# Kernel tuning notes

Measured on AMD Instinct MI355X. Metric: run time of the kernel, lower is better.

## Reference

```python
import jax, jax.numpy as jnp
import numpy as np

N, E, G = 50000, 800000, 64
H, C, EDIM = 4, 64, 16
NT, NR, NCLS = 8, 6, 2
NEG_SLOPE = 0.2


def setup_inputs() -> dict:
    key = jax.random.key(0)
    ks = jax.random.split(key, 24)
    d = {}
    d['node_type'] = jax.random.randint(ks[0], (N,), 0, NT, dtype=jnp.int32)
    d['edge_type'] = jax.random.randint(ks[1], (E,), 0, NR, dtype=jnp.int32)
    d['edge_index'] = jax.random.randint(ks[2], (2, E), 0, N, dtype=jnp.int32)
    d['batch'] = jnp.sort(jax.random.randint(ks[3], (N,), 0, G, dtype=jnp.int32))
    i = [4]
    def rn(shape, scale=0.1):
        a = jax.random.normal(ks[i[0]], shape, dtype=jnp.float32) * scale
        i[0] += 1
        return a
    d['node_emb'] = rn((NT, C))
    d['edge_emb'] = rn((NR, EDIM))
    for l in (0, 1):
        d[f'W{l}'] = rn((C, H * C))
        d[f'We{l}'] = rn((EDIM, H * C))
        d[f'att_src{l}'] = rn((H, C))
        d[f'att_dst{l}'] = rn((H, C))
        d[f'att_edge{l}'] = rn((H, C))
        d[f'b{l}'] = jnp.zeros((C,), jnp.float32)
    d['cw1'] = rn((C, C))
    d['cb1'] = jnp.zeros((C,), jnp.float32)
    d['cw2'] = rn((C, NCLS))
    d['cb2'] = jnp.zeros((NCLS,), jnp.float32)
    return d


def gat_layer(x, ea, src, dst, W, We, a_src, a_dst, a_edge, b):
    # x: [N, C], ea: [E, EDIM]
    h = (x @ W).reshape(N, H, C)          # transformed node features
    he = (ea @ We).reshape(E, H, C)       # transformed edge features
    # per-edge attention logits [E, H]
    alpha = ((h * a_src).sum(-1)[src]
             + (h * a_dst).sum(-1)[dst]
             + (he * a_edge).sum(-1))
    alpha = jax.nn.leaky_relu(alpha, NEG_SLOPE)
    # segment softmax over destination neighborhoods
    m = jax.ops.segment_max(alpha, dst, num_segments=N)
    alpha = jnp.exp(alpha - m[dst])
    den = jax.ops.segment_sum(alpha, dst, num_segments=N)
    alpha = alpha / (den[dst] + 1e-16)
    # weighted scatter-add of source features, then mean over heads
    out = jax.ops.segment_sum(alpha[:, :, None] * h[src], dst, num_segments=N)
    return jax.nn.elu(out.mean(axis=1) + b)


def reference(node_type, edge_type, edge_index, batch, node_emb, edge_emb,
              W0, We0, att_src0, att_dst0, att_edge0, b0,
              W1, We1, att_src1, att_dst1, att_edge1, b1,
              cw1, cb1, cw2, cb2):
    src, dst = edge_index[0], edge_index[1]
    x = node_emb[node_type]          # [N, C]
    ea = edge_emb[edge_type]         # [E, EDIM]
    x = gat_layer(x, ea, src, dst, W0, We0, att_src0, att_dst0, att_edge0, b0)
    x = gat_layer(x, ea, src, dst, W1, We1, att_src1, att_dst1, att_edge1, b1)
    # global mean pool over graphs
    s = jax.ops.segment_sum(x, batch, num_segments=G)
    cnt = jax.ops.segment_sum(jnp.ones((N, 1), x.dtype), batch, num_segments=G)
    g = s / jnp.maximum(cnt, 1.0)
    # classifier (dropout inactive in eval)
    return jax.nn.relu(g @ cw1 + cb1) @ cw2 + cb2
```

## Files before the change

kernel.cpp:

```cpp
#include <hip/hip_runtime.h>
#include <hip/hip_bf16.h>

#define N_NODES 50000
#define N_EDGES 800000
#define N_GRAPH 64
#define NHEAD 4
#define CDIM 64
#define HC 256
#define NTT 8
#define NRR 6
#define EDIMM 16
#define SCAN_CHUNK 1024
#define NBLK_SCAN ((N_NODES + SCAN_CHUNK - 1) / SCAN_CHUNK)
#define H1SCALE 1024.f

typedef unsigned short u16;
typedef unsigned char u8;
typedef __attribute__((ext_vector_type(8))) short bf8;
typedef __attribute__((ext_vector_type(4))) float f4;
typedef __attribute__((ext_vector_type(2))) float v2f;

__device__ __forceinline__ float eluf(float v) { return v > 0.f ? v : expm1f(v); }
__device__ __forceinline__ u16 f2u(float f) {
    union { float f; unsigned int i; } c; c.f = f;
    unsigned int i = c.i;
    return (u16)((i + 0x7FFFu + ((i >> 16) & 1u)) >> 16);
}
__device__ __forceinline__ float lrelu(float v) { return v > 0.f ? v : 0.2f * v; }
__device__ __forceinline__ u8 f2fp8(float v) {
    return (u8)(__builtin_amdgcn_cvt_pk_fp8_f32(v, 0.f, 0, false) & 0xFF);
}

__global__ __launch_bounds__(256) void k_zero(float* __restrict__ p, int n)
{
    int i = blockIdx.x * 256 + threadIdx.x;
    if (i < n) p[i] = 0.f;
}

__global__ __launch_bounds__(256) void k_tables(
    const float* __restrict__ node_emb, const float* __restrict__ edge_emb,
    const float* __restrict__ W0, const float* __restrict__ We0,
    const float* __restrict__ as0, const float* __restrict__ ad0,
    const float* __restrict__ ae0, const float* __restrict__ We1,
    const float* __restrict__ ae1,
    float* __restrict__ t_h0, float* __restrict__ t_as0,
    float* __restrict__ t_ad0, float* __restrict__ t_ae0,
    float* __restrict__ t_ae1)
{
    __shared__ float srow[HC];
    __shared__ float srow2[HC];
    int tid = threadIdx.x;
    int b = blockIdx.x;
    if (b < NTT) {
        int t = b;
        float acc = 0.f;
        #pragma unroll 8
        for (int k = 0; k < CDIM; k++)
            acc += node_emb[t * CDIM + k] * W0[k * HC + tid];
        srow[tid] = acc;
        t_h0[t * HC + tid] = acc;
        __syncthreads();
        if (tid < NHEAD) {
            int h = tid;
            float a = 0.f, d = 0.f;
            for (int c = 0; c < CDIM; c++) {
                float hv = srow[h * CDIM + c];
                a += hv * as0[h * CDIM + c];
                d += hv * ad0[h * CDIM + c];
            }
            t_as0[t * NHEAD + h] = a;
            t_ad0[t * NHEAD + h] = d;
        }
    } else {
        int r = b - NTT;
        float a0 = 0.f, a1 = 0.f;
        #pragma unroll
        for (int k = 0; k < EDIMM; k++) {
            float ev = edge_emb[r * EDIMM + k];
            a0 += ev * We0[k * HC + tid];
            a1 += ev * We1[k * HC + tid];
        }
        srow[tid] = a0;
        srow2[tid] = a1;
        __syncthreads();
        if (tid < NHEAD) {
            int h = tid;
            float s0 = 0.f, s1 = 0.f;
            for (int c = 0; c < CDIM; c++) {
                s0 += srow[h * CDIM + c] * ae0[h * CDIM + c];
                s1 += srow2[h * CDIM + c] * ae1[h * CDIM + c];
            }
            t_ae0[r * NHEAD + h] = s0;
            t_ae1[r * NHEAD + h] = s1;
        }
    }
}

__global__ __launch_bounds__(256) void k_exptab(
    const float* __restrict__ t_as0, const float* __restrict__ t_ad0,
    const float* __restrict__ t_ae0, float* __restrict__ t_exp)
{
    for (int idx = threadIdx.x; idx < NTT * NRR * NTT * NHEAD; idx += 256) {
        int tn = idx / 192;
        int rem = idx - tn * 192;
        int et = rem >> 5;
        int ts = (rem >> 2) & 7;
        int h = rem & 3;
        float lg = t_as0[ts * NHEAD + h] + t_ad0[tn * NHEAD + h]
                 + t_ae0[et * NHEAD + h];
        t_exp[idx] = __expf(lrelu(lg));
    }
}

__global__ __launch_bounds__(256) void k_count(
    const int* __restrict__ edge_index, int* __restrict__ deg4,
    const int* __restrict__ batch, int* __restrict__ goffs)
{
    int i = blockIdx.x * 256 + threadIdx.x;
    if (i < N_EDGES)
        atomicAdd(&deg4[(blockIdx.x & 3) * N_NODES + edge_index[N_EDGES + i]], 1);
    if (i < N_NODES) {
        int bi = batch[i];
        int bp = (i == 0) ? -1 : batch[i - 1];
        for (int g = bp + 1; g <= bi; g++) goffs[g] = i;
        if (i == N_NODES - 1)
            for (int g = bi + 1; g <= N_GRAPH; g++) goffs[g] = N_NODES;
    }
}

__global__ __launch_bounds__(256) void k_scan1(
    const int* __restrict__ deg4, int* __restrict__ deg, int* __restrict__ blksum)
{
    __shared__ int s[256];
    int b = blockIdx.x, tid = threadIdx.x;
    int base = b * SCAN_CHUNK + tid * 4;
    int t = 0;
    #pragma unroll
    for (int k = 0; k < 4; k++) {
        int i = base + k;
        if (i < N_NODES) {
            int d = deg4[i] + deg4[N_NODES + i] + deg4[2 * N_NODES + i]
                  + deg4[3 * N_NODES + i];
            deg[i] = d;
            t += d;
        }
    }
    s[tid] = t;
    __syncthreads();
    for (int off = 128; off > 0; off >>= 1) {
        if (tid < off) s[tid] += s[tid + off];
        __syncthreads();
    }
    if (tid == 0) blksum[b] = s[0];
}

__global__ __launch_bounds__(256) void k_scan3(
    const int* __restrict__ deg, const int* __restrict__ blksum,
    int* __restrict__ offs, int* __restrict__ cursor)
{
    __shared__ int s[256];
    __shared__ int sbase;
    int b = blockIdx.x, tid = threadIdx.x;
    if (tid < 64) {
        int v = (tid < b) ? blksum[tid] : 0;
        #pragma unroll
        for (int d = 32; d >= 1; d >>= 1) v += __shfl_xor(v, d);
        if (tid == 0) sbase = v;
    }
    int base = b * SCAN_CHUNK + tid * 4;
    int d4[4]; int t = 0;
    #pragma unroll
    for (int k = 0; k < 4; k++) {
        int i = base + k;
        d4[k] = (i < N_NODES) ? deg[i] : 0;
        t += d4[k];
    }
    s[tid] = t;
    __syncthreads();
    for (int off = 1; off < 256; off <<= 1) {
        int v = (tid >= off) ? s[tid - off] : 0;
        __syncthreads();
        s[tid] += v;
        __syncthreads();
    }
    int excl = sbase + s[tid] - t;
    #pragma unroll
    for (int k = 0; k < 4; k++) {
        int i = base + k;
        if (i < N_NODES) { offs[i] = excl; cursor[i] = excl; }
        excl += d4[k];
    }
    if (b == NBLK_SCAN - 1 && tid == 255) offs[N_NODES] = excl;
}

__global__ __launch_bounds__(256) void k_scatter(
    const int* __restrict__ edge_index, const int* __restrict__ edge_type,
    const int* __restrict__ node_type, int* __restrict__ cursor,
    int* __restrict__ csrp)
{
    int e = blockIdx.x * 256 + threadIdx.x;
    if (e < N_EDGES) {
        int d  = edge_index[N_EDGES + e];
        int s  = edge_index[e];
        int et = edge_type[e];
        int ts = node_type[s];
        int pos = atomicAdd(&cursor[d], 1);
        csrp[pos] = s | (et << 16) | (ts << 19);
    }
}

__global__ __launch_bounds__(256) void k_layer0(
    const int* __restrict__ node_type, const int* __restrict__ offs,
    const int* __restrict__ csrp,
    const float* __restrict__ t_h0, const float* __restrict__ t_exp,
    const float* __restrict__ b0, u16* __restrict__ x1b)
{
    __shared__ float s_h0[NTT * HC];
    __shared__ float s_exp[NTT * NRR * NTT * NHEAD];
    __shared__ float s_b0[CDIM];

    int tid = threadIdx.x;
    for (int i = tid; i < NTT * HC; i += 256) s_h0[i] = t_h0[i];
    for (int i = tid; i < NTT * NRR * NTT * NHEAD; i += 256) s_exp[i] = t_exp[i];
    if (tid < CDIM) s_b0[tid] = b0[tid];
    __syncthreads();

    int n = (blockIdx.x * 256 + tid) >> 6;
    int lane = tid & 63;
    int h = lane >> 4;
    int cq = (lane & 15) << 2;
    int hoff = h * CDIM + cq;

    int tnbase = node_type[n] * 192 + h;
    int e0 = offs[n], e1 = offs[n + 1];
    int efull = e0 + ((e1 - e0) & ~3);
    float ax = 0.f, ay = 0.f, az = 0.f, aw = 0.f, den = 0.f;
    for (int i = e0; i < efull; i += 4) {
        int rA = csrp[i],     rB = csrp[i + 1];
        int rC = csrp[i + 2], rD = csrp[i + 3];
        int tA = rA >> 19, tB = rB >> 19, tC = rC >> 19, tD = rD >> 19;
        int eA = (rA >> 16) & 7, eB = (rB >> 16) & 7;
        int eC = (rC >> 16) & 7, eD = (rD >> 16) & 7;
        float pA = s_exp[tnbase + (eA << 5) + (tA << 2)];
        float pB = s_exp[tnbase + (eB << 5) + (tB << 2)];
        float pC = s_exp[tnbase + (eC << 5) + (tC << 2)];
        float pD = s_exp[tnbase + (eD << 5) + (tD << 2)];
        den += pA + pB + pC + pD;
        const float4 vA = *(const float4*)(s_h0 + tA * HC + hoff);
        const float4 vB = *(const float4*)(s_h0 + tB * HC + hoff);
        const float4 vC = *(const float4*)(s_h0 + tC * HC + hoff);
        const float4 vD = *(const float4*)(s_h0 + tD * HC + hoff);
        ax += pA * vA.x + pB * vB.x + pC * vC.x + pD * vD.x;
        ay += pA * vA.y + pB * vB.y + pC * vC.y + pD * vD.y;
        az += pA * vA.z + pB * vB.z + pC * vC.z + pD * vD.z;
        aw += pA * vA.w + pB * vB.w + pC * vC.w + pD * vD.w;
    }
    for (int i = efull; i < e1; i++) {
        int r = csrp[i];
        int ts = r >> 19, et = (r >> 16) & 7;
        float p = s_exp[tnbase + (et << 5) + (ts << 2)];
        den += p;
        const float4 v = *(const float4*)(s_h0 + ts * HC + hoff);
        ax += p * v.x; ay += p * v.y; az += p * v.z; aw += p * v.w;
    }
    float inv = 0.25f / (den + 1e-16f);
    ax *= inv; ay *= inv; az *= inv; aw *= inv;
    ax += __shfl_xor(ax, 16); ax += __shfl_xor(ax, 32);
    ay += __shfl_xor(ay, 16); ay += __shfl_xor(ay, 32);
    az += __shfl_xor(az, 16); az += __shfl_xor(az, 32);
    aw += __shfl_xor(aw, 16); aw += __shfl_xor(aw, 32);
    if (lane < 16) {
        ushort4 o;
        o.x = f2u(eluf(ax + s_b0[cq + 0]));
        o.y = f2u(eluf(ay + s_b0[cq + 1]));
        o.z = f2u(eluf(az + s_b0[cq + 2]));
        o.w = f2u(eluf(aw + s_b0[cq + 3]));
        *(ushort4*)(x1b + (size_t)n * CDIM + cq) = o;
    }
}

__global__ __launch_bounds__(256) void k_gemm1(
    const u16* __restrict__ x1b, const float* __restrict__ W1,
    const float* __restrict__ as1, const float* __restrict__ ad1,
    u8* __restrict__ h1f8, float* __restrict__ asrc1, float* __restrict__ adst1)
{
    __shared__ u8 ht[16 * HC];
    int tid = threadIdx.x;
    int lane = tid & 63, wv = tid >> 6;
    int quad = lane >> 4, c16 = lane & 15;

    bf8 bf[4][2];
    float sv[4], dv[4];
    #pragma unroll
    for (int t = 0; t < 4; t++) {
        int col = wv * 64 + t * 16 + c16;
        sv[t] = as1[col];
        dv[t] = ad1[col];
        #pragma unroll
        for (int kf = 0; kf < 2; kf++)
            #pragma unroll
            for (int j = 0; j < 8; j++)
                bf[t][kf][j] = (short)f2u(W1[(kf * 32 + quad * 8 + j) * HC + col]);
    }

    for (int it = 0; it < 5; it++) {
        int nt = it * 625 + blockIdx.x;
        const bf8 a0 = *(const bf8*)(x1b + (size_t)(nt * 16 + c16) * CDIM + quad * 8);
        const bf8 a1 = *(const bf8*)(x1b + (size_t)(nt * 16 + c16) * CDIM + 32 + quad * 8);
        f4 acc[4];
        #pragma unroll
        for (int t = 0; t < 4; t++) {
            acc[t] = (f4){0.f, 0.f, 0.f, 0.f};
            acc[t] = __builtin_amdgcn_mfma_f32_16x16x32_bf16(a0, bf[t][0], acc[t], 0, 0, 0);
            acc[t] = __builtin_amdgcn_mfma_f32_16x16x32_bf16(a1, bf[t][1], acc[t], 0, 0, 0);
        }
        float rs[4] = {0.f, 0.f, 0.f, 0.f}, rd[4] = {0.f, 0.f, 0.f, 0.f};
        #pragma unroll
        for (int t = 0; t < 4; t++)
            #pragma unroll
            for (int reg = 0; reg < 4; reg++) {
                float v = acc[t][reg];
                rs[reg] += v * sv[t];
                rd[reg] += v * dv[t];
                ht[(quad * 4 + reg) * HC + wv * 64 + t * 16 + c16] = f2fp8(v * H1SCALE);
            }
        #pragma unroll
        for (int reg = 0; reg < 4; reg++)
            #pragma unroll
            for (int d = 1; d < 16; d <<= 1) {
                rs[reg] += __shfl_xor(rs[reg], d);
                rd[reg] += __shfl_xor(rd[reg], d);
            }
        if (c16 == 0) {
            #pragma unroll
            for (int reg = 0; reg < 4; reg++) {
                int n = nt * 16 + quad * 4 + reg;
                asrc1[n * NHEAD + wv] = rs[reg];
                adst1[n * NHEAD + wv] = rd[reg];
            }
        }
        __syncthreads();
        const uint4* src = (const uint4*)ht;
        uint4* dst = (uint4*)(h1f8 + (size_t)nt * 16 * HC);
        dst[tid] = src[tid];
        __syncthreads();
    }
}

__global__ __launch_bounds__(256) void k_agg1(
    const int* __restrict__ offs, const int* __restrict__ csrp,
    const u8* __restrict__ h1f8, const float* __restrict__ asrc1,
    const float* __restrict__ adst1, const float* __restrict__ t_ae1,
    const float* __restrict__ b1, float* __restrict__ x2)
{
    __shared__ float s_ae[NRR * NHEAD];
    if (threadIdx.x < NRR * NHEAD) s_ae[threadIdx.x] = t_ae1[threadIdx.x];
    __syncthreads();

    int n = (blockIdx.x * 256 + threadIdx.x) >> 6;
    int lane = threadIdx.x & 63;
    int h = lane >> 4;
    int cq = (lane & 15) << 2;
    float adst = adst1[n * NHEAD + h];
    int e0 = offs[n], e1 = offs[n + 1];
    int efull = e0 + ((e1 - e0) & ~7);

    float ax = 0.f, ay = 0.f, az = 0.f, aw = 0.f, den = 0.f;
    for (int i = e0; i < efull; i += 8) {
        int rec[8], s[8], et[8];
        #pragma unroll
        for (int k = 0; k < 8; k++) rec[k] = csrp[i + k];
        #pragma unroll
        for (int k = 0; k < 8; k++) { s[k] = rec[k] & 0xFFFF; et[k] = (rec[k] >> 16) & 7; }
        float asv[8];
        unsigned int hw[8];
        #pragma unroll
        for (int k = 0; k < 8; k++) asv[k] = asrc1[s[k] * NHEAD + h];
        #pragma unroll
        for (int k = 0; k < 8; k++)
            hw[k] = *(const unsigned int*)(h1f8 + (size_t)s[k] * HC + h * CDIM + cq);
        #pragma unroll
        for (int k = 0; k < 8; k++) {
            float p = __expf(lrelu(asv[k] + adst + s_ae[et[k] * NHEAD + h]));
            den += p;
            v2f lo = __builtin_amdgcn_cvt_pk_f32_fp8(hw[k], false);
            v2f hi = __builtin_amdgcn_cvt_pk_f32_fp8(hw[k], true);
            ax += p * lo.x; ay += p * lo.y;
            az += p * hi.x; aw += p * hi.y;
        }
    }
    for (int i = efull; i < e1; i++) {
        int rec = csrp[i];
        int s = rec & 0xFFFF, et = (rec >> 16) & 7;
        float p = __expf(lrelu(asrc1[s * NHEAD + h] + adst + s_ae[et * NHEAD + h]));
        den += p;
        unsigned int w = *(const unsigned int*)(h1f8 + (size_t)s * HC + h * CDIM + cq);
        v2f lo = __builtin_amdgcn_cvt_pk_f32_fp8(w, false);
        v2f hi = __builtin_amdgcn_cvt_pk_f32_fp8(w, true);
        ax += p * lo.x; ay += p * lo.y;
        az += p * hi.x; aw += p * hi.y;
    }
    float inv = (0.25f / H1SCALE) / (den + 1e-16f);
    ax *= inv; ay *= inv; az *= inv; aw *= inv;
    ax += __shfl_xor(ax, 16); ax += __shfl_xor(ax, 32);
    ay += __shfl_xor(ay, 16); ay += __shfl_xor(ay, 32);
    az += __shfl_xor(az, 16); az += __shfl_xor(az, 32);
    aw += __shfl_xor(aw, 16); aw += __shfl_xor(aw, 32);
    if (lane < 16) {
        float4 o;
        o.x = eluf(ax + b1[cq + 0]);
        o.y = eluf(ay + b1[cq + 1]);
        o.z = eluf(az + b1[cq + 2]);
        o.w = eluf(aw + b1[cq + 3]);
        *(float4*)(x2 + (size_t)n * CDIM + cq) = o;
    }
}

__global__ __launch_bounds__(256) void k_poolcls(
    const float* __restrict__ x2, const int* __restrict__ goffs,
    const float* __restrict__ cw1, const float* __restrict__ cb1,
    const float* __restrict__ cw2, const float* __restrict__ cb2,
    float* __restrict__ out, int wsMB,
    const int* __restrict__ offs, const int* __restrict__ csrp,
    const float* __restrict__ W1)
{
    __shared__ float part[4][CDIM];
    __shared__ float gsh[CDIM];
    int g = blockIdx.x;
    int ch = threadIdx.x & 63, rg = threadIdx.x >> 6;
    int gs = goffs[g], ge = goffs[g + 1];
    float acc = 0.f;
    for (int r = gs + rg; r < ge; r += 4)
        acc += x2[(size_t)r * CDIM + ch];
    part[rg][ch] = acc;
    __syncthreads();
    if (threadIdx.x < CDIM) {
        float s = part[0][ch] + part[1][ch] + part[2][ch] + part[3][ch];
        int c = ge - gs;
        gsh[ch] = s / (float)(c > 1 ? c : 1);
    }
    __syncthreads();
    if (threadIdx.x < 64) {
        int j = threadIdx.x;
        float a = cb1[j];
        #pragma unroll
        for (int k = 0; k < CDIM; k++) a += gsh[k] * cw1[k * CDIM + j];
        float hid = a > 0.f ? a : 0.f;
        float o0 = hid * cw2[j * 2 + 0];
        float o1 = hid * cw2[j * 2 + 1];
        #pragma unroll
        for (int d = 32; d >= 1; d >>= 1) {
            o0 += __shfl_xor(o0, d);
            o1 += __shfl_xor(o1, d);
        }
        if (j == 0) {
            out[g * 2 + 0] = o0 + cb2[0];
            out[g * 2 + 1] = o1 + cb2[1];
        }
    }
    if (g == 0) {
        __shared__ int simpl, soob, sA;
        if (threadIdx.x == 0) { simpl = 0; soob = 0; sA = 0; }
        __syncthreads();
        if (threadIdx.x == 0 && offs[N_NODES] != N_EDGES) atomicOr(&sA, 4);
        float v = W1[threadIdx.x];
        if (!(fabsf(v) < 100.f)) atomicAdd(&simpl, 1);
        int r = csrp[threadIdx.x];
        if ((r & 0xFFFF) >= N_NODES || (r >> 22) != 0 || r < 0) atomicAdd(&soob, 1);
        __syncthreads();
        if (threadIdx.x == 0) {
            int A = sA;
            if (simpl > 10) A |= 8;
            int B = soob > 1023 ? 1023 : soob;
            if (A | B) out[0] = (float)((A << 20) | (wsMB << 10) | B);
        }
    }
}

__global__ void k_fault(int code, float* __restrict__ out)
{
    if (threadIdx.x == 0 && blockIdx.x == 0) out[0] = (float)code;
}

extern "C" void kernel_launch(void* const* d_in, const int* in_sizes, int n_in,
                              void* d_out, int out_size, void* d_ws, size_t ws_size,
                              hipStream_t stream) {
    static const int rsize[22] = {50000, 800000, 1600000, 50000, 512, 96,
                                  16384, 4096, 256, 256, 256, 64,
                                  16384, 4096, 256, 256, 256, 64,
                                  4096, 64, 128, 2};
    static const int cand_pos[3][22] = {
        {21,19,18,12,20,17,0,2,8,4,6,10,1,3,9,5,7,11,15,13,16,14},
        {0,1,2,3,4,5,6,7,8,9,10,11,12,13,14,15,16,17,18,19,20,21},
        {17,15,14,8,16,13,18,20,4,0,2,6,19,21,5,1,3,7,11,9,12,10},
    };
    int mc = -1;
    if (n_in == 22) {
        for (int c = 0; c < 3 && mc < 0; c++) {
            bool ok = true;
            for (int r = 0; r < 22; r++)
                if (in_sizes[cand_pos[c][r]] != rsize[r]) { ok = false; break; }
            if (ok) mc = c;
        }
    }

    char* ws = (char*)d_ws;
    size_t off = 0;
    auto alloc = [&](size_t b) { size_t r = off; off += (b + 255) & ~(size_t)255; return r; };
    int*   deg4   = (int*)(ws + alloc((size_t)4 * N_NODES * 4));
    size_t zero_bytes = off;
    int*   deg    = (int*)(ws + alloc(N_NODES * 4));
    int*   blksum = (int*)(ws + alloc(NBLK_SCAN * 4));
    int*   offs   = (int*)(ws + alloc((N_NODES + 1) * 4));
    int*   cursor = (int*)(ws + alloc(N_NODES * 4));
    int*   csrp   = (int*)(ws + alloc(N_EDGES * 4));
    int*   goffs  = (int*)(ws + alloc((N_GRAPH + 1) * 4));
    float* t_h0   = (float*)(ws + alloc(NTT * HC * 4));
    float* t_as0  = (float*)(ws + alloc(NTT * NHEAD * 4));
    float* t_ad0  = (float*)(ws + alloc(NTT * NHEAD * 4));
    float* t_ae0  = (float*)(ws + alloc(NRR * NHEAD * 4));
    float* t_ae1  = (float*)(ws + alloc(NRR * NHEAD * 4));
    float* t_exp  = (float*)(ws + alloc(NTT * NRR * NTT * NHEAD * 4));
    u16*   x1b    = (u16*)(ws + alloc((size_t)N_NODES * CDIM * 2));
    float* asrc1  = (float*)(ws + alloc((size_t)N_NODES * NHEAD * 4));
    float* adst1  = (float*)(ws + alloc((size_t)N_NODES * NHEAD * 4));
    u8*    h1f8   = (u8*)(ws + alloc((size_t)N_NODES * HC));
    float* x2     = (float*)(ws + alloc((size_t)N_NODES * CDIM * 4));

    int wsMB = (int)(ws_size >> 20); if (wsMB > 1023) wsMB = 1023;
    int hostA = 0, hostB = 0;
    if (mc < 0) { hostA |= 1; hostB = (n_in != 22) ? (n_in < 1023 ? n_in : 1023) : 0; }
    if (mc >= 0 && off > ws_size) hostA |= 2;

    if (hostA == 0) {
        const int* P = cand_pos[mc];
        const int*   node_type  = (const int*)d_in[P[0]];
        const int*   edge_type  = (const int*)d_in[P[1]];
        const int*   edge_index = (const int*)d_in[P[2]];
        const int*   batch      = (const int*)d_in[P[3]];
        const float* node_emb   = (const float*)d_in[P[4]];
        const float* edge_emb   = (const float*)d_in[P[5]];
        const float* W0  = (const float*)d_in[P[6]];
        const float* We0 = (const float*)d_in[P[7]];
        const float* as0 = (const float*)d_in[P[8]];
        const float* ad0 = (const float*)d_in[P[9]];
        const float* ae0 = (const float*)d_in[P[10]];
        const float* b0  = (const float*)d_in[P[11]];
        const float* W1  = (const float*)d_in[P[12]];
        const float* We1 = (const float*)d_in[P[13]];
        const float* as1 = (const float*)d_in[P[14]];
        const float* ad1 = (const float*)d_in[P[15]];
        const float* ae1 = (const float*)d_in[P[16]];
        const float* b1  = (const float*)d_in[P[17]];
        const float* cw1 = (const float*)d_in[P[18]];
        const float* cb1 = (const float*)d_in[P[19]];
        const float* cw2 = (const float*)d_in[P[20]];
        const float* cb2 = (const float*)d_in[P[21]];

        int zero_elems = (int)(zero_bytes / 4);
        k_zero<<<(zero_elems + 255) / 256, 256, 0, stream>>>((float*)ws, zero_elems);
        k_tables<<<NTT + NRR, 256, 0, stream>>>(node_emb, edge_emb, W0, We0, as0,
                                                ad0, ae0, We1, ae1,
                                                t_h0, t_as0, t_ad0, t_ae0, t_ae1);
        k_exptab<<<1, 256, 0, stream>>>(t_as0, t_ad0, t_ae0, t_exp);
        k_count<<<(N_EDGES + 255) / 256, 256, 0, stream>>>(edge_index, deg4,
                                                           batch, goffs);
        k_scan1<<<NBLK_SCAN, 256, 0, stream>>>(deg4, deg, blksum);
        k_scan3<<<NBLK_SCAN, 256, 0, stream>>>(deg, blksum, offs, cursor);
        k_scatter<<<(N_EDGES + 255) / 256, 256, 0, stream>>>(edge_index, edge_type,
                                                             node_type, cursor, csrp);
        k_layer0<<<(N_NODES * 64) / 256, 256, 0, stream>>>(
            node_type, offs, csrp, t_h0, t_exp, b0, x1b);
        k_gemm1<<<625, 256, 0, stream>>>(
            x1b, W1, as1, ad1, h1f8, asrc1, adst1);
        k_agg1<<<(N_NODES * 64) / 256, 256, 0, stream>>>(
            offs, csrp, h1f8, asrc1, adst1, t_ae1, b1, x2);
        k_poolcls<<<N_GRAPH, 256, 0, stream>>>(
            x2, goffs, cw1, cb1, cw2, cb2, (float*)d_out, wsMB, offs, csrp, W1);
    } else {
        int code = (hostA << 20) | (wsMB << 10) | (hostB > 1023 ? 1023 : hostB);
        k_fault<<<1, 64, 0, stream>>>(code, (float*)d_out);
    }
}
```

Before: 348.7 us.

## Fuse exp table into layer0, prefetch CSR records, distribute attention exps across lanes

Result: no change. 354.8 us (+1.8%).

```diff
diff --git a/kernel.cpp b/kernel.cpp
--- a/kernel.cpp
+++ b/kernel.cpp
@@ -96,22 +96,6 @@
     }
 }
 
-__global__ __launch_bounds__(256) void k_exptab(
-    const float* __restrict__ t_as0, const float* __restrict__ t_ad0,
-    const float* __restrict__ t_ae0, float* __restrict__ t_exp)
-{
-    for (int idx = threadIdx.x; idx < NTT * NRR * NTT * NHEAD; idx += 256) {
-        int tn = idx / 192;
-        int rem = idx - tn * 192;
-        int et = rem >> 5;
-        int ts = (rem >> 2) & 7;
-        int h = rem & 3;
-        float lg = t_as0[ts * NHEAD + h] + t_ad0[tn * NHEAD + h]
-                 + t_ae0[et * NHEAD + h];
-        t_exp[idx] = __expf(lrelu(lg));
-    }
-}
-
 __global__ __launch_bounds__(256) void k_count(
     const int* __restrict__ edge_index, int* __restrict__ deg4,
     const int* __restrict__ batch, int* __restrict__ goffs)
@@ -212,17 +196,35 @@
 __global__ __launch_bounds__(256) void k_layer0(
     const int* __restrict__ node_type, const int* __restrict__ offs,
     const int* __restrict__ csrp,
-    const float* __restrict__ t_h0, const float* __restrict__ t_exp,
+    const float* __restrict__ t_h0,
+    const float* __restrict__ t_as0, const float* __restrict__ t_ad0,
+    const float* __restrict__ t_ae0,
     const float* __restrict__ b0, u16* __restrict__ x1b)
 {
     __shared__ float s_h0[NTT * HC];
     __shared__ float s_exp[NTT * NRR * NTT * NHEAD];
     __shared__ float s_b0[CDIM];
+    __shared__ float s_att[2 * NTT * NHEAD + NRR * NHEAD];
 
     int tid = threadIdx.x;
     for (int i = tid; i < NTT * HC; i += 256) s_h0[i] = t_h0[i];
-    for (int i = tid; i < NTT * NRR * NTT * NHEAD; i += 256) s_exp[i] = t_exp[i];
+    if (tid < NTT * NHEAD) s_att[tid] = t_as0[tid];
+    else if (tid < 2 * NTT * NHEAD) s_att[tid] = t_ad0[tid - NTT * NHEAD];
+    else if (tid < 2 * NTT * NHEAD + NRR * NHEAD)
+        s_att[tid] = t_ae0[tid - 2 * NTT * NHEAD];
     if (tid < CDIM) s_b0[tid] = b0[tid];
+    __syncthreads();
+    for (int idx = tid; idx < NTT * NRR * NTT * NHEAD; idx += 256) {
+        int tn = idx / 192;
+        int rem = idx - tn * 192;
+        int et = rem >> 5;
+        int ts = (rem >> 2) & 7;
+        int hq = idx & 3;
+        float lg = s_att[ts * NHEAD + hq]
+                 + s_att[NTT * NHEAD + tn * NHEAD + hq]
+                 + s_att[2 * NTT * NHEAD + et * NHEAD + hq];
+        s_exp[idx] = __expf(lrelu(lg));
+    }
     __syncthreads();
 
     int n = (blockIdx.x * 256 + tid) >> 6;
@@ -233,35 +235,37 @@
 
     int tnbase = node_type[n] * 192 + h;
     int e0 = offs[n], e1 = offs[n + 1];
-    int efull = e0 + ((e1 - e0) & ~3);
+    int nb = (e1 - e0 + 7) >> 3;
     float ax = 0.f, ay = 0.f, az = 0.f, aw = 0.f, den = 0.f;
-    for (int i = e0; i < efull; i += 4) {
-        int rA = csrp[i],     rB = csrp[i + 1];
-        int rC = csrp[i + 2], rD = csrp[i + 3];
-        int tA = rA >> 19, tB = rB >> 19, tC = rC >> 19, tD = rD >> 19;
-        int eA = (rA >> 16) & 7, eB = (rB >> 16) & 7;
-        int eC = (rC >> 16) & 7, eD = (rD >> 16) & 7;
-        float pA = s_exp[tnbase + (eA << 5) + (tA << 2)];
-        float pB = s_exp[tnbase + (eB << 5) + (tB << 2)];
-        float pC = s_exp[tnbase + (eC << 5) + (tC << 2)];
-        float pD = s_exp[tnbase + (eD << 5) + (tD << 2)];
-        den += pA + pB + pC + pD;
-        const float4 vA = *(const float4*)(s_h0 + tA * HC + hoff);
-        const float4 vB = *(const float4*)(s_h0 + tB * HC + hoff);
-        const float4 vC = *(const float4*)(s_h0 + tC * HC + hoff);
-        const float4 vD = *(const float4*)(s_h0 + tD * HC + hoff);
-        ax += pA * vA.x + pB * vB.x + pC * vC.x + pD * vD.x;
-        ay += pA * vA.y + pB * vB.y + pC * vC.y + pD * vD.y;
-        az += pA * vA.z + pB * vB.z + pC * vC.z + pD * vD.z;
-        aw += pA * vA.w + pB * vB.w + pC * vC.w + pD * vD.w;
-    }
-    for (int i = efull; i < e1; i++) {
-        int r = csrp[i];
-        int ts = r >> 19, et = (r >> 16) & 7;
-        float p = s_exp[tnbase + (et << 5) + (ts << 2)];
-        den += p;
-        const float4 v = *(const float4*)(s_h0 + ts * HC + hoff);
-        ax += p * v.x; ay += p * v.y; az += p * v.z; aw += p * v.w;
+
+    int rec[8];
+    if (nb > 0) {
+        #pragma unroll
+        for (int k = 0; k < 8; k++) {
+            int idx = e0 + k; idx = idx < e1 ? idx : e1 - 1;
+            rec[k] = csrp[idx];
+        }
+    }
+    for (int b = 0; b < nb; b++) {
+        int i = e0 + (b << 3);
+        int lim = e1 - i;
+        int ts8[8], et8[8];
+        #pragma unroll
+        for (int k = 0; k < 8; k++) { ts8[k] = rec[k] >> 19; et8[k] = (rec[k] >> 16) & 7; }
+        int ii = i + 8;
+        #pragma unroll
+        for (int k = 0; k < 8; k++) {
+            int idx = ii + k; idx = idx < e1 ? idx : e1 - 1;
+            rec[k] = csrp[idx];
+        }
+        #pragma unroll
+        for (int k = 0; k < 8; k++) {
+            float p = s_exp[tnbase + (et8[k] << 5) + (ts8[k] << 2)];
+            p = (k < lim) ? p : 0.f;
+            den += p;
+            const float4 v = *(const float4*)(s_h0 + ts8[k] * HC + hoff);
+            ax += p * v.x; ay += p * v.y; az += p * v.z; aw += p * v.w;
+        }
     }
     float inv = 0.25f / (den + 1e-16f);
     ax *= inv; ay *= inv; az *= inv; aw *= inv;
@@ -303,48 +307,45 @@
                 bf[t][kf][j] = (short)f2u(W1[(kf * 32 + quad * 8 + j) * HC + col]);
     }
 
-    for (int it = 0; it < 5; it++) {
-        int nt = it * 625 + blockIdx.x;
-        const bf8 a0 = *(const bf8*)(x1b + (size_t)(nt * 16 + c16) * CDIM + quad * 8);
-        const bf8 a1 = *(const bf8*)(x1b + (size_t)(nt * 16 + c16) * CDIM + 32 + quad * 8);
-        f4 acc[4];
-        #pragma unroll
-        for (int t = 0; t < 4; t++) {
-            acc[t] = (f4){0.f, 0.f, 0.f, 0.f};
-            acc[t] = __builtin_amdgcn_mfma_f32_16x16x32_bf16(a0, bf[t][0], acc[t], 0, 0, 0);
-            acc[t] = __builtin_amdgcn_mfma_f32_16x16x32_bf16(a1, bf[t][1], acc[t], 0, 0, 0);
-        }
-        float rs[4] = {0.f, 0.f, 0.f, 0.f}, rd[4] = {0.f, 0.f, 0.f, 0.f};
-        #pragma unroll
-        for (int t = 0; t < 4; t++)
-            #pragma unroll
-            for (int reg = 0; reg < 4; reg++) {
-                float v = acc[t][reg];
-                rs[reg] += v * sv[t];
-                rd[reg] += v * dv[t];
-                ht[(quad * 4 + reg) * HC + wv * 64 + t * 16 + c16] = f2fp8(v * H1SCALE);
-            }
-        #pragma unroll
-        for (int reg = 0; reg < 4; reg++)
-            #pragma unroll
-            for (int d = 1; d < 16; d <<= 1) {
-                rs[reg] += __shfl_xor(rs[reg], d);
-                rd[reg] += __shfl_xor(rd[reg], d);
-            }
-        if (c16 == 0) {
-            #pragma unroll
-            for (int reg = 0; reg < 4; reg++) {
-                int n = nt * 16 + quad * 4 + reg;
-                asrc1[n * NHEAD + wv] = rs[reg];
-                adst1[n * NHEAD + wv] = rd[reg];
-            }
-        }
-        __syncthreads();
-        const uint4* src = (const uint4*)ht;
-        uint4* dst = (uint4*)(h1f8 + (size_t)nt * 16 * HC);
-        dst[tid] = src[tid];
-        __syncthreads();
-    }
+    int nt = blockIdx.x;
+    const bf8 a0 = *(const bf8*)(x1b + (size_t)(nt * 16 + c16) * CDIM + quad * 8);
+    const bf8 a1 = *(const bf8*)(x1b + (size_t)(nt * 16 + c16) * CDIM + 32 + quad * 8);
+    f4 acc[4];
+    #pragma unroll
+    for (int t = 0; t < 4; t++) {
+        acc[t] = (f4){0.f, 0.f, 0.f, 0.f};
+        acc[t] = __builtin_amdgcn_mfma_f32_16x16x32_bf16(a0, bf[t][0], acc[t], 0, 0, 0);
+        acc[t] = __builtin_amdgcn_mfma_f32_16x16x32_bf16(a1, bf[t][1], acc[t], 0, 0, 0);
+    }
+    float rs[4] = {0.f, 0.f, 0.f, 0.f}, rd[4] = {0.f, 0.f, 0.f, 0.f};
+    #pragma unroll
+    for (int t = 0; t < 4; t++)
+        #pragma unroll
+        for (int reg = 0; reg < 4; reg++) {
+            float v = acc[t][reg];
+            rs[reg] += v * sv[t];
+            rd[reg] += v * dv[t];
+            ht[(quad * 4 + reg) * HC + wv * 64 + t * 16 + c16] = f2fp8(v * H1SCALE);
+        }
+    #pragma unroll
+    for (int reg = 0; reg < 4; reg++)
+        #pragma unroll
+        for (int d = 1; d < 16; d <<= 1) {
+            rs[reg] += __shfl_xor(rs[reg], d);
+            rd[reg] += __shfl_xor(rd[reg], d);
+        }
+    if (c16 == 0) {
+        #pragma unroll
+        for (int reg = 0; reg < 4; reg++) {
+            int nn = nt * 16 + quad * 4 + reg;
+            asrc1[nn * NHEAD + wv] = rs[reg];
+            adst1[nn * NHEAD + wv] = rd[reg];
+        }
+    }
+    __syncthreads();
+    const uint4* src = (const uint4*)ht;
+    uint4* dst = (uint4*)(h1f8 + (size_t)nt * 16 * HC);
+    dst[tid] = src[tid];
 }
 
 __global__ __launch_bounds__(256) void k_agg1(
@@ -361,44 +362,53 @@
     int lane = threadIdx.x & 63;
     int h = lane >> 4;
     int cq = (lane & 15) << 2;
-    float adst = adst1[n * NHEAD + h];
+    int q  = lane & 31;
+    int ke = q >> 2;
+    int hh = q & 3;
+    float adst_hh = adst1[n * NHEAD + hh];
+
     int e0 = offs[n], e1 = offs[n + 1];
-    int efull = e0 + ((e1 - e0) & ~7);
+    int nb = (e1 - e0 + 7) >> 3;
 
     float ax = 0.f, ay = 0.f, az = 0.f, aw = 0.f, den = 0.f;
-    for (int i = e0; i < efull; i += 8) {
-        int rec[8], s[8], et[8];
-        #pragma unroll
-        for (int k = 0; k < 8; k++) rec[k] = csrp[i + k];
-        #pragma unroll
-        for (int k = 0; k < 8; k++) { s[k] = rec[k] & 0xFFFF; et[k] = (rec[k] >> 16) & 7; }
-        float asv[8];
+
+    int rec[8];
+    if (nb > 0) {
+        #pragma unroll
+        for (int k = 0; k < 8; k++) {
+            int idx = e0 + k; idx = idx < e1 ? idx : e1 - 1;
+            rec[k] = csrp[idx];
+        }
+    }
+    for (int b = 0; b < nb; b++) {
+        int i = e0 + (b << 3);
+        int lim = e1 - i;
+        int s[8];
+        #pragma unroll
+        for (int k = 0; k < 8; k++) s[k] = rec[k] & 0xFFFF;
+        int ete = (rec[ke] >> 16) & 7;
+        float asve = asrc1[s[ke] * NHEAD + hh];
         unsigned int hw[8];
-        #pragma unroll
-        for (int k = 0; k < 8; k++) asv[k] = asrc1[s[k] * NHEAD + h];
         #pragma unroll
         for (int k = 0; k < 8; k++)
             hw[k] = *(const unsigned int*)(h1f8 + (size_t)s[k] * HC + h * CDIM + cq);
+        int ii = i + 8;
         #pragma unroll
         for (int k = 0; k < 8; k++) {
-            float p = __expf(lrelu(asv[k] + adst + s_ae[et[k] * NHEAD + h]));
+            int idx = ii + k; idx = idx < e1 ? idx : e1 - 1;
+            rec[k] = csrp[idx];
+        }
+        float pe = __expf(lrelu(asve + adst_hh + s_ae[ete * NHEAD + hh]));
+        #pragma unroll
+        for (int k = 0; k < 8; k++) {
+            float p = __shfl(pe, (k << 2) | h);
+            p = (k < lim) ? p : 0.f;
             den += p;
             v2f lo = __builtin_amdgcn_cvt_pk_f32_fp8(hw[k], false);
             v2f hi = __builtin_amdgcn_cvt_pk_f32_fp8(hw[k], true);
             ax += p * lo.x; ay += p * lo.y;
             az += p * hi.x; aw += p * hi.y;
         }
-    }
-    for (int i = efull; i < e1; i++) {
-        int rec = csrp[i];
-        int s = rec & 0xFFFF, et = (rec >> 16) & 7;
-        float p = __expf(lrelu(asrc1[s * NHEAD + h] + adst + s_ae[et * NHEAD + h]));
-        den += p;
-        unsigned int w = *(const unsigned int*)(h1f8 + (size_t)s * HC + h * CDIM + cq);
-        v2f lo = __builtin_amdgcn_cvt_pk_f32_fp8(w, false);
-        v2f hi = __builtin_amdgcn_cvt_pk_f32_fp8(w, true);
-        ax += p * lo.x; ay += p * lo.y;
-        az += p * hi.x; aw += p * hi.y;
     }
     float inv = (0.25f / H1SCALE) / (den + 1e-16f);
     ax *= inv; ay *= inv; az *= inv; aw *= inv;
@@ -520,7 +530,6 @@
     float* t_ad0  = (float*)(ws + alloc(NTT * NHEAD * 4));
     float* t_ae0  = (float*)(ws + alloc(NRR * NHEAD * 4));
     float* t_ae1  = (float*)(ws + alloc(NRR * NHEAD * 4));
-    float* t_exp  = (float*)(ws + alloc(NTT * NRR * NTT * NHEAD * 4));
     u16*   x1b    = (u16*)(ws + alloc((size_t)N_NODES * CDIM * 2));
     float* asrc1  = (float*)(ws + alloc((size_t)N_NODES * NHEAD * 4));
     float* adst1  = (float*)(ws + alloc((size_t)N_NODES * NHEAD * 4));
@@ -562,7 +571,6 @@
         k_tables<<<NTT + NRR, 256, 0, stream>>>(node_emb, edge_emb, W0, We0, as0,
                                                 ad0, ae0, We1, ae1,
                                                 t_h0, t_as0, t_ad0, t_ae0, t_ae1);
-        k_exptab<<<1, 256, 0, stream>>>(t_as0, t_ad0, t_ae0, t_exp);
         k_count<<<(N_EDGES + 255) / 256, 256, 0, stream>>>(edge_index, deg4,
                                                            batch, goffs);
         k_scan1<<<NBLK_SCAN, 256, 0, stream>>>(deg4, deg, blksum);
@@ -570,8 +578,8 @@
         k_scatter<<<(N_EDGES + 255) / 256, 256, 0, stream>>>(edge_index, edge_type,
                                                              node_type, cursor, csrp);
         k_layer0<<<(N_NODES * 64) / 256, 256, 0, stream>>>(
-            node_type, offs, csrp, t_h0, t_exp, b0, x1b);
-        k_gemm1<<<625, 256, 0, stream>>>(
+            node_type, offs, csrp, t_h0, t_as0, t_ad0, t_ae0, b0, x1b);
+        k_gemm1<<<3125, 256, 0, stream>>>(
             x1b, W1, as1, ad1, h1f8, asrc1, adst1);
         k_agg1<<<(N_NODES * 64) / 256, 256, 0, stream>>>(
             offs, csrp, h1f8, asrc1, adst1, t_ae1, b1, x2);
```
